# Optimization experiments

Measured on AMD Instinct MI355X. Metric: run time of the kernel, lower is better.

The kernel has to match this reference:

```python
import jax, jax.numpy as jnp
import numpy as np

N = 262144          # nodes
E = N * 16          # edges (avg degree 16)
C_IN = 64
C_OUT = 64
GRID = 0.5          # voxel size
POS_EXTENT = 10.0   # pos in [0, 10)^3
NVOX_DIM = int(round(POS_EXTENT / GRID))  # 20
NVOX = NVOX_DIM ** 3                      # 8000 voxels
BN_EPS = 1e-5


def setup_inputs() -> dict:
    key = jax.random.key(0)
    k = jax.random.split(key, 5)
    x = jax.random.normal(k[0], (N, C_IN), dtype=jnp.float32)
    pos = jax.random.uniform(k[1], (N, 3), dtype=jnp.float32, minval=0.0, maxval=POS_EXTENT)
    edge_index = jax.random.randint(k[2], (2, E), 0, N, dtype=jnp.int32)
    W = jax.random.normal(k[3], (C_IN, C_OUT), dtype=jnp.float32) / np.float32(np.sqrt(C_IN))
    b = jnp.zeros((C_OUT,), jnp.float32)
    gamma = jnp.ones((C_OUT,), jnp.float32)
    beta = jnp.zeros((C_OUT,), jnp.float32)
    return {"x": x, "pos": pos, "edge_index": edge_index,
            "W": W, "b": b, "gamma": gamma, "beta": beta}


def reference(x, pos, edge_index, W, b, gamma, beta):
    # --- self.down: Linear -> BatchNorm1d (training-mode batch stats) -> ReLU ---
    h = x @ W + b                                   # [N, C_OUT]
    mean = jnp.mean(h, axis=0)
    var = jnp.mean(jnp.square(h - mean), axis=0)    # biased variance (torch BN)
    h = (h - mean) * jax.lax.rsqrt(var + BN_EPS) * gamma + beta
    h = jax.nn.relu(h)

    # --- max_pool_neighbor_x: scatter-max of neighbor features (self-loops added) ---
    row, col = edge_index[0], edge_index[1]
    pooled = jax.ops.segment_max(h[row], col, num_segments=N)  # [N, C_OUT]
    h = jnp.maximum(pooled, h)  # self-loop; also fixes -inf for isolated nodes

    # --- GridSampling: voxel-grid quantize + per-voxel mean of x and pos ---
    vid = jnp.clip(jnp.floor(pos / GRID).astype(jnp.int32), 0, NVOX_DIM - 1)  # [N,3]
    vox = (vid[:, 0] * NVOX_DIM + vid[:, 1]) * NVOX_DIM + vid[:, 2]           # [N]
    cnt = jax.ops.segment_sum(jnp.ones((N,), jnp.float32), vox, num_segments=NVOX)
    x_sum = jax.ops.segment_sum(h, vox, num_segments=NVOX)     # [NVOX, C_OUT]
    p_sum = jax.ops.segment_sum(pos, vox, num_segments=NVOX)   # [NVOX, 3]
    denom = jnp.maximum(cnt, 1.0)[:, None]
    x_out = x_sum / denom
    pos_out = p_sum / denom
    # concat features and positions of the downsampled graph: [NVOX, C_OUT+3]
    return jnp.concatenate([x_out, pos_out], axis=1)
```

## Files before the change

### kernel.cpp

```cpp
#include <hip/hip_runtime.h>
#include <hip/hip_fp16.h>

#define NVOX_DIM 20
#define NVOX 8000
#define BN_EPS 1e-5f

#define NBUCK 2048
#define BSHIFT 7
#define NODES_PER_BUCK 128
#define GEMM_BLOCKS 1024
#define ZERO_BLOCKS 16
#define CAP 2560

typedef _Float16 f16x8 __attribute__((ext_vector_type(8)));
typedef float f32x4 __attribute__((ext_vector_type(4)));

__device__ __forceinline__ unsigned short f2key(float v) {
    unsigned short hb = __half_as_ushort(__float2half(v));
    unsigned short m = (unsigned short)(0x8000u | (unsigned short)(-(int)(hb >> 15)));
    return (unsigned short)(hb ^ m);
}

__global__ __launch_bounds__(256) void k0_fused(const float* __restrict__ x,
                                                const float* __restrict__ W,
                                                const float* __restrict__ bias,
                                                unsigned short* __restrict__ h16,
                                                float* __restrict__ partials, int n16,
                                                float4* __restrict__ zero_zone,
                                                int zero_n4) {
    __shared__ float sW[4096];
    __shared__ float red[2][4][64];
    int t = threadIdx.x;

    if (blockIdx.x >= GEMM_BLOCKS) {
        int zb = blockIdx.x - GEMM_BLOCKS;
        float4 z = {0.f, 0.f, 0.f, 0.f};
        for (int i = zb * 256 + t; i < zero_n4; i += ZERO_BLOCKS * 256) zero_zone[i] = z;
        return;
    }

    for (int i = t; i < 4096; i += 256) sW[i] = W[i];
    __syncthreads();
    int lane = t & 63;
    int w = t >> 6;
    int l15 = lane & 15;
    int q = lane >> 4;

    f16x8 bf[4][2];
#pragma unroll
    for (int t4 = 0; t4 < 4; ++t4)
#pragma unroll
        for (int kb = 0; kb < 2; ++kb)
#pragma unroll
            for (int i = 0; i < 8; ++i)
                bf[t4][kb][i] = (_Float16)sW[(kb * 32 + q * 8 + i) * 64 + t4 * 16 + l15];
    float bv[4];
#pragma unroll
    for (int t4 = 0; t4 < 4; ++t4) bv[t4] = bias[t4 * 16 + l15];

    float s[4] = {0.f, 0.f, 0.f, 0.f}, s2[4] = {0.f, 0.f, 0.f, 0.f};

    for (int g = blockIdx.x * 4 + w; g < n16; g += GEMM_BLOCKS * 4) {
        int row0 = g * 16;
        const float* xp = x + (size_t)(row0 + l15) * 64 + q * 8;
        float4 xa = *(const float4*)(xp);
        float4 xb = *(const float4*)(xp + 4);
        float4 xc = *(const float4*)(xp + 32);
        float4 xd = *(const float4*)(xp + 36);
        f16x8 a0, a1;
        a0[0] = (_Float16)xa.x; a0[1] = (_Float16)xa.y; a0[2] = (_Float16)xa.z; a0[3] = (_Float16)xa.w;
        a0[4] = (_Float16)xb.x; a0[5] = (_Float16)xb.y; a0[6] = (_Float16)xb.z; a0[7] = (_Float16)xb.w;
        a1[0] = (_Float16)xc.x; a1[1] = (_Float16)xc.y; a1[2] = (_Float16)xc.z; a1[3] = (_Float16)xc.w;
        a1[4] = (_Float16)xd.x; a1[5] = (_Float16)xd.y; a1[6] = (_Float16)xd.z; a1[7] = (_Float16)xd.w;

#pragma unroll
        for (int t4 = 0; t4 < 4; ++t4) {
            f32x4 acc = {bv[t4], bv[t4], bv[t4], bv[t4]};
            acc = __builtin_amdgcn_mfma_f32_16x16x32_f16(a0, bf[t4][0], acc, 0, 0, 0);
            acc = __builtin_amdgcn_mfma_f32_16x16x32_f16(a1, bf[t4][1], acc, 0, 0, 0);
            s[t4] += acc[0] + acc[1] + acc[2] + acc[3];
            s2[t4] = fmaf(acc[0], acc[0], s2[t4]);
            s2[t4] = fmaf(acc[1], acc[1], s2[t4]);
            s2[t4] = fmaf(acc[2], acc[2], s2[t4]);
            s2[t4] = fmaf(acc[3], acc[3], s2[t4]);
#pragma unroll
            for (int r = 0; r < 4; ++r) {
                h16[(size_t)(row0 + q * 4 + r) * 64 + t4 * 16 + l15] = f2key(acc[r]);
            }
        }
    }

#pragma unroll
    for (int t4 = 0; t4 < 4; ++t4) {
        s[t4] += __shfl_xor(s[t4], 16, 64);
        s[t4] += __shfl_xor(s[t4], 32, 64);
        s2[t4] += __shfl_xor(s2[t4], 16, 64);
        s2[t4] += __shfl_xor(s2[t4], 32, 64);
    }
    if (lane < 16) {
#pragma unroll
        for (int t4 = 0; t4 < 4; ++t4) {
            red[0][w][t4 * 16 + lane] = s[t4];
            red[1][w][t4 * 16 + lane] = s2[t4];
        }
    }
    __syncthreads();
    if (t < 128) {
        int c = t & 63;
        int which = t >> 6;
        float v = red[which][0][c] + red[which][1][c] + red[which][2][c] + red[which][3][c];
        partials[(size_t)blockIdx.x * 128 + which * 64 + c] = v;
    }
}

__global__ __launch_bounds__(1024) void k3_finalize(const float* __restrict__ partials,
                                                    const float* __restrict__ gamma,
                                                    const float* __restrict__ beta,
                                                    float* __restrict__ stats2, float invN) {
    __shared__ float red[8][128];
    __shared__ float tot[128];
    int t = threadIdx.x;
    int c = t & 127;
    int g = t >> 7;
    float s = 0.f;
    for (int b = g; b < GEMM_BLOCKS; b += 8) s += partials[(size_t)b * 128 + c];
    red[g][c] = s;
    __syncthreads();
    if (t < 128) {
        float v = 0.f;
#pragma unroll
        for (int g2 = 0; g2 < 8; ++g2) v += red[g2][t];
        tot[t] = v;
    }
    __syncthreads();
    if (t < 64) {
        float mean = tot[t] * invN;
        float var = tot[64 + t] * invN - mean * mean;
        float sc = gamma[t] * rsqrtf(var + BN_EPS);
        stats2[t] = sc;
        stats2[64 + t] = beta[t] - mean * sc;
    }
}

__global__ __launch_bounds__(1024) void k_bin(const int* __restrict__ rows,
                                              const int* __restrict__ cols,
                                              int* __restrict__ cursor,
                                              unsigned int* __restrict__ pairs, int E) {
    __shared__ int lh[NBUCK];
    __shared__ int lpos[NBUCK];
    int t = threadIdx.x;
    lh[t] = 0;
    lh[t + 1024] = 0;
    __syncthreads();
    int base = blockIdx.x * 16384 + t * 16;
    int r[16], c[16];
#pragma unroll
    for (int g4 = 0; g4 < 4; ++g4) {
        int e = base + g4 * 4;
        int4 r4 = *(const int4*)(rows + e);
        int4 c4 = *(const int4*)(cols + e);
        r[g4 * 4 + 0] = r4.x; c[g4 * 4 + 0] = c4.x;
        r[g4 * 4 + 1] = r4.y; c[g4 * 4 + 1] = c4.y;
        r[g4 * 4 + 2] = r4.z; c[g4 * 4 + 2] = c4.z;
        r[g4 * 4 + 3] = r4.w; c[g4 * 4 + 3] = c4.w;
    }
#pragma unroll
    for (int i = 0; i < 16; ++i) atomicAdd(&lh[c[i] >> BSHIFT], 1);
    __syncthreads();
    lpos[t] = atomicAdd(&cursor[t], lh[t]);
    lpos[t + 1024] = atomicAdd(&cursor[t + 1024], lh[t + 1024]);
    __syncthreads();
#pragma unroll
    for (int i = 0; i < 16; ++i) {
        int bkt = c[i] >> BSHIFT;
        int idx = atomicAdd(&lpos[bkt], 1);
        if (idx < CAP)
            pairs[(size_t)bkt * CAP + idx] =
                ((unsigned int)r[i] << BSHIFT) |
                (unsigned int)(c[i] & (NODES_PER_BUCK - 1));
    }
}

__global__ __launch_bounds__(512) void k_pool(const unsigned int* __restrict__ pairs,
                                              const int* __restrict__ cursor,
                                              const unsigned short* __restrict__ h16,
                                              const float* __restrict__ pos,
                                              const float* __restrict__ stats2,
                                              float* __restrict__ xs,
                                              float* __restrict__ ps,
                                              float* __restrict__ cnt) {
    __shared__ unsigned int tile[NODES_PER_BUCK * 64];
    int b = blockIdx.x;
    int t = threadIdx.x;
    int lane = t & 63;
    int w = t >> 6;
    float scale = stats2[lane];
    float shift = stats2[64 + lane];

    const unsigned int* src = (const unsigned int*)(h16 + (size_t)b * (NODES_PER_BUCK * 64));
#pragma unroll
    for (int k = 0; k < 8; ++k) {
        int i = t + k * 512;
        unsigned int u = src[i];
        tile[2 * i] = u & 0xFFFFu;
        tile[2 * i + 1] = u >> 16;
    }
    __syncthreads();

    int cntE = min(__builtin_amdgcn_readfirstlane(cursor[b]), CAP);
    int chunk = (((cntE + 7) >> 3) + 7) & ~7;
    int wu = __builtin_amdgcn_readfirstlane(w);
    int start = b * CAP;
    int cs = start + wu * chunk;
    int ce = min(cs + chunk, start + cntE);
    int j = cs;
    for (; j + 16 <= ce; j += 16) {
        uint4 qa = *(const uint4*)(pairs + j);
        uint4 qb = *(const uint4*)(pairs + j + 4);
        uint4 qc = *(const uint4*)(pairs + j + 8);
        uint4 qd = *(const uint4*)(pairs + j + 12);
        unsigned int v0 = h16[(size_t)(qa.x >> BSHIFT) * 64 + lane];
        unsigned int v1 = h16[(size_t)(qa.y >> BSHIFT) * 64 + lane];
        unsigned int v2 = h16[(size_t)(qa.z >> BSHIFT) * 64 + lane];
        unsigned int v3 = h16[(size_t)(qa.w >> BSHIFT) * 64 + lane];
        unsigned int v4 = h16[(size_t)(qb.x >> BSHIFT) * 64 + lane];
        unsigned int v5 = h16[(size_t)(qb.y >> BSHIFT) * 64 + lane];
        unsigned int v6 = h16[(size_t)(qb.z >> BSHIFT) * 64 + lane];
        unsigned int v7 = h16[(size_t)(qb.w >> BSHIFT) * 64 + lane];
        unsigned int v8 = h16[(size_t)(qc.x >> BSHIFT) * 64 + lane];
        unsigned int v9 = h16[(size_t)(qc.y >> BSHIFT) * 64 + lane];
        unsigned int va = h16[(size_t)(qc.z >> BSHIFT) * 64 + lane];
        unsigned int vb = h16[(size_t)(qc.w >> BSHIFT) * 64 + lane];
        unsigned int vc = h16[(size_t)(qd.x >> BSHIFT) * 64 + lane];
        unsigned int vd = h16[(size_t)(qd.y >> BSHIFT) * 64 + lane];
        unsigned int ve = h16[(size_t)(qd.z >> BSHIFT) * 64 + lane];
        unsigned int vf = h16[(size_t)(qd.w >> BSHIFT) * 64 + lane];
        const unsigned int M = NODES_PER_BUCK - 1;
        atomicMax(&tile[((qa.x & M) << 6) + lane], v0);
        atomicMax(&tile[((qa.y & M) << 6) + lane], v1);
        atomicMax(&tile[((qa.z & M) << 6) + lane], v2);
        atomicMax(&tile[((qa.w & M) << 6) + lane], v3);
        atomicMax(&tile[((qb.x & M) << 6) + lane], v4);
        atomicMax(&tile[((qb.y & M) << 6) + lane], v5);
        atomicMax(&tile[((qb.z & M) << 6) + lane], v6);
        atomicMax(&tile[((qb.w & M) << 6) + lane], v7);
        atomicMax(&tile[((qc.x & M) << 6) + lane], v8);
        atomicMax(&tile[((qc.y & M) << 6) + lane], v9);
        atomicMax(&tile[((qc.z & M) << 6) + lane], va);
        atomicMax(&tile[((qc.w & M) << 6) + lane], vb);
        atomicMax(&tile[((qd.x & M) << 6) + lane], vc);
        atomicMax(&tile[((qd.y & M) << 6) + lane], vd);
        atomicMax(&tile[((qd.z & M) << 6) + lane], ve);
        atomicMax(&tile[((qd.w & M) << 6) + lane], vf);
    }
    for (; j < ce; ++j) {
        unsigned int qq = __builtin_amdgcn_readfirstlane(pairs[j]);
        unsigned int v = h16[(size_t)(qq >> BSHIFT) * 64 + lane];
        atomicMax(&tile[((qq & (NODES_PER_BUCK - 1)) << 6) + lane], v);
    }
    __syncthreads();

#pragma unroll
    for (int nl = 0; nl < NODES_PER_BUCK; nl += 8) {
        int node_l = nl + w;
        int c = (b << BSHIFT) + node_l;
        float px = pos[(size_t)c * 3 + 0];
        float py = pos[(size_t)c * 3 + 1];
        float pz = pos[(size_t)c * 3 + 2];
        int v0 = min(max((int)floorf(px * 2.f), 0), NVOX_DIM - 1);
        int v1 = min(max((int)floorf(py * 2.f), 0), NVOX_DIM - 1);
        int v2 = min(max((int)floorf(pz * 2.f), 0), NVOX_DIM - 1);
        int vox = (v0 * NVOX_DIM + v1) * NVOX_DIM + v2;
        unsigned int k = tile[(node_l << 6) + lane];
        unsigned short hb = (k & 0x8000u) ? (unsigned short)(k ^ 0x8000u)
                                          : (unsigned short)(0xFFFFu ^ k);
        __half_raw hr;
        hr.x = hb;
        float v = __half2float((__half)hr);
        float val = fmaxf(fmaf(v, scale, shift), 0.f);
        atomicAdd(&xs[(size_t)vox * 64 + lane], val);
        if (lane < 3) atomicAdd(&ps[vox * 3 + lane], lane == 0 ? px : (lane == 1 ? py : pz));
        if (lane == 0) atomicAdd(&cnt[vox], 1.f);
    }
}

__global__ __launch_bounds__(256) void k7_out(const float* __restrict__ xs,
                                              const float* __restrict__ ps,
                                              const float* __restrict__ cnt,
                                              float* __restrict__ out, int total) {
    int idx = blockIdx.x * blockDim.x + threadIdx.x;
    if (idx >= total) return;
    int v = idx / 67;
    int c = idx - v * 67;
    float d = fmaxf(cnt[v], 1.f);
    float val = (c < 64) ? xs[(size_t)v * 64 + c] : ps[v * 3 + (c - 64)];
    out[idx] = val / d;
}

extern "C" void kernel_launch(void* const* d_in, const int* in_sizes, int n_in,
                              void* d_out, int out_size, void* d_ws, size_t ws_size,
                              hipStream_t stream) {
    const float* x     = (const float*)d_in[0];
    const float* pos   = (const float*)d_in[1];
    const int*   ei    = (const int*)d_in[2];
    const float* W     = (const float*)d_in[3];
    const float* b     = (const float*)d_in[4];
    const float* gamma = (const float*)d_in[5];
    const float* beta  = (const float*)d_in[6];
    float* out = (float*)d_out;

    const int n = in_sizes[0] / 64;
    const int E = in_sizes[2] / 2;

    char* ws = (char*)d_ws;
    unsigned short* h16      = (unsigned short*)(ws + 0);
    unsigned int*   pairs    = (unsigned int*)(ws + 33554432);
    float*          partials = (float*)(ws + 54525952);
    float*          stats2   = (float*)(ws + 55050240);
    int*            cursor   = (int*)(ws + 55051264);
    float*          xs       = (float*)(ws + 55059456);
    float*          ps       = (float*)(ws + 57107456);
    float*          cnt      = (float*)(ws + 57203456);
    float4*         zero4    = (float4*)(ws + 55059456);
    const int zero_n4 = (57235456 - 55059456) / 16;

    hipMemsetAsync(cursor, 0, NBUCK * 4, stream);

    k0_fused<<<GEMM_BLOCKS + ZERO_BLOCKS, 256, 0, stream>>>(x, W, b, h16, partials,
                                                            n >> 4, zero4, zero_n4);
    k_bin<<<E / 16384, 1024, 0, stream>>>(ei, ei + E, cursor, pairs, E);
    k3_finalize<<<1, 1024, 0, stream>>>(partials, gamma, beta, stats2, 1.0f / (float)n);
    k_pool<<<NBUCK, 512, 0, stream>>>(pairs, cursor, h16, pos, stats2, xs, ps, cnt);
    k7_out<<<(out_size + 255) / 256, 256, 0, stream>>>(xs, ps, cnt, out, out_size);
}
```

Measured before the change: 357.6 us.

## Replace voxel atomic scatter with per-voxel node lists and gather reduction

Nodes are binned into fixed-capacity per-voxel lists inside the edge-binning kernel. The pooling kernel now writes pooled fp16 keys to a buffer. A new per-voxel kernel then gathers those keys, applies BN and ReLU, and writes the averaged output directly. This removes float atomics to the voxel sums, the zeroing pass and the final divide kernel. Edge buckets also grow to 256 nodes with 1024-thread pool blocks. Two risks: the CAPV=96 limit silently drops nodes in crowded voxels (the mean is about 33 per voxel), and pooled results make an extra round trip through memory.

New measurement: 350.4 us. 2.0% less time.

```diff
diff --git a/kernel.cpp b/kernel.cpp
--- a/kernel.cpp
+++ b/kernel.cpp
@@ -5,12 +5,13 @@
 #define NVOX 8000
 #define BN_EPS 1e-5f
 
-#define NBUCK 2048
-#define BSHIFT 7
-#define NODES_PER_BUCK 128
+#define NBUCK 1024
+#define BSHIFT 8
+#define NODES_PER_BUCK 256
 #define GEMM_BLOCKS 1024
-#define ZERO_BLOCKS 16
-#define CAP 2560
+#define CAP 5120
+#define CAPV 96
+#define NODEBIN_BLOCKS 32
 
 typedef _Float16 f16x8 __attribute__((ext_vector_type(8)));
 typedef float f32x4 __attribute__((ext_vector_type(4)));
@@ -21,24 +22,22 @@
     return (unsigned short)(hb ^ m);
 }
 
-__global__ __launch_bounds__(256) void k0_fused(const float* __restrict__ x,
-                                                const float* __restrict__ W,
-                                                const float* __restrict__ bias,
-                                                unsigned short* __restrict__ h16,
-                                                float* __restrict__ partials, int n16,
-                                                float4* __restrict__ zero_zone,
-                                                int zero_n4) {
+__device__ __forceinline__ float key2f(unsigned int k) {
+    unsigned short hb = (k & 0x8000u) ? (unsigned short)(k ^ 0x8000u)
+                                      : (unsigned short)(0xFFFFu ^ k);
+    __half_raw hr;
+    hr.x = hb;
+    return __half2float((__half)hr);
+}
+
+__global__ __launch_bounds__(256) void k0_gemm(const float* __restrict__ x,
+                                               const float* __restrict__ W,
+                                               const float* __restrict__ bias,
+                                               unsigned short* __restrict__ h16,
+                                               float* __restrict__ partials, int n16) {
     __shared__ float sW[4096];
     __shared__ float red[2][4][64];
     int t = threadIdx.x;
-
-    if (blockIdx.x >= GEMM_BLOCKS) {
-        int zb = blockIdx.x - GEMM_BLOCKS;
-        float4 z = {0.f, 0.f, 0.f, 0.f};
-        for (int i = zb * 256 + t; i < zero_n4; i += ZERO_BLOCKS * 256) zero_zone[i] = z;
-        return;
-    }
-
     for (int i = t; i < 4096; i += 256) sW[i] = W[i];
     __syncthreads();
     int lane = t & 63;
@@ -144,13 +143,35 @@
 
 __global__ __launch_bounds__(1024) void k_bin(const int* __restrict__ rows,
                                               const int* __restrict__ cols,
-                                              int* __restrict__ cursor,
-                                              unsigned int* __restrict__ pairs, int E) {
+                                              const float* __restrict__ pos,
+                                              int* __restrict__ cursorE,
+                                              unsigned int* __restrict__ pairs,
+                                              int* __restrict__ cursorV,
+                                              int* __restrict__ vox_nodes,
+                                              int E, int n) {
     __shared__ int lh[NBUCK];
     __shared__ int lpos[NBUCK];
     int t = threadIdx.x;
+
+    if (blockIdx.x >= 256) {
+        int nb = blockIdx.x - 256;
+#pragma unroll
+        for (int i = 0; i < 8; ++i) {
+            int node = nb * 8192 + i * 1024 + t;
+            float px = pos[(size_t)node * 3 + 0];
+            float py = pos[(size_t)node * 3 + 1];
+            float pz = pos[(size_t)node * 3 + 2];
+            int v0 = min(max((int)floorf(px * 2.f), 0), NVOX_DIM - 1);
+            int v1 = min(max((int)floorf(py * 2.f), 0), NVOX_DIM - 1);
+            int v2 = min(max((int)floorf(pz * 2.f), 0), NVOX_DIM - 1);
+            int vox = (v0 * NVOX_DIM + v1) * NVOX_DIM + v2;
+            int idx = atomicAdd(&cursorV[vox], 1);
+            if (idx < CAPV) vox_nodes[vox * CAPV + idx] = node;
+        }
+        return;
+    }
+
     lh[t] = 0;
-    lh[t + 1024] = 0;
     __syncthreads();
     int base = blockIdx.x * 16384 + t * 16;
     int r[16], c[16];
@@ -167,8 +188,7 @@
 #pragma unroll
     for (int i = 0; i < 16; ++i) atomicAdd(&lh[c[i] >> BSHIFT], 1);
     __syncthreads();
-    lpos[t] = atomicAdd(&cursor[t], lh[t]);
-    lpos[t + 1024] = atomicAdd(&cursor[t + 1024], lh[t + 1024]);
+    lpos[t] = atomicAdd(&cursorE[t], lh[t]);
     __syncthreads();
 #pragma unroll
     for (int i = 0; i < 16; ++i) {
@@ -181,39 +201,34 @@
     }
 }
 
-__global__ __launch_bounds__(512) void k_pool(const unsigned int* __restrict__ pairs,
-                                              const int* __restrict__ cursor,
-                                              const unsigned short* __restrict__ h16,
-                                              const float* __restrict__ pos,
-                                              const float* __restrict__ stats2,
-                                              float* __restrict__ xs,
-                                              float* __restrict__ ps,
-                                              float* __restrict__ cnt) {
+__global__ __launch_bounds__(1024) void k_pool(const unsigned int* __restrict__ pairs,
+                                               const int* __restrict__ cursorE,
+                                               const unsigned short* __restrict__ h16,
+                                               unsigned short* __restrict__ pooled16) {
     __shared__ unsigned int tile[NODES_PER_BUCK * 64];
     int b = blockIdx.x;
     int t = threadIdx.x;
     int lane = t & 63;
     int w = t >> 6;
-    float scale = stats2[lane];
-    float shift = stats2[64 + lane];
 
     const unsigned int* src = (const unsigned int*)(h16 + (size_t)b * (NODES_PER_BUCK * 64));
 #pragma unroll
     for (int k = 0; k < 8; ++k) {
-        int i = t + k * 512;
+        int i = t + k * 1024;
         unsigned int u = src[i];
         tile[2 * i] = u & 0xFFFFu;
         tile[2 * i + 1] = u >> 16;
     }
     __syncthreads();
 
-    int cntE = min(__builtin_amdgcn_readfirstlane(cursor[b]), CAP);
-    int chunk = (((cntE + 7) >> 3) + 7) & ~7;
+    int cntE = min(__builtin_amdgcn_readfirstlane(cursorE[b]), CAP);
+    int chunk = (((cntE + 15) >> 4) + 7) & ~7;
     int wu = __builtin_amdgcn_readfirstlane(w);
     int start = b * CAP;
     int cs = start + wu * chunk;
     int ce = min(cs + chunk, start + cntE);
     int j = cs;
+    const unsigned int M = NODES_PER_BUCK - 1;
     for (; j + 16 <= ce; j += 16) {
         uint4 qa = *(const uint4*)(pairs + j);
         uint4 qb = *(const uint4*)(pairs + j + 4);
@@ -235,7 +250,6 @@
         unsigned int vd = h16[(size_t)(qd.y >> BSHIFT) * 64 + lane];
         unsigned int ve = h16[(size_t)(qd.z >> BSHIFT) * 64 + lane];
         unsigned int vf = h16[(size_t)(qd.w >> BSHIFT) * 64 + lane];
-        const unsigned int M = NODES_PER_BUCK - 1;
         atomicMax(&tile[((qa.x & M) << 6) + lane], v0);
         atomicMax(&tile[((qa.y & M) << 6) + lane], v1);
         atomicMax(&tile[((qa.z & M) << 6) + lane], v2);
@@ -256,45 +270,63 @@
     for (; j < ce; ++j) {
         unsigned int qq = __builtin_amdgcn_readfirstlane(pairs[j]);
         unsigned int v = h16[(size_t)(qq >> BSHIFT) * 64 + lane];
-        atomicMax(&tile[((qq & (NODES_PER_BUCK - 1)) << 6) + lane], v);
-    }
-    __syncthreads();
-
-#pragma unroll
-    for (int nl = 0; nl < NODES_PER_BUCK; nl += 8) {
+        atomicMax(&tile[((qq & M) << 6) + lane], v);
+    }
+    __syncthreads();
+
+#pragma unroll
+    for (int nl = 0; nl < NODES_PER_BUCK; nl += 16) {
         int node_l = nl + w;
-        int c = (b << BSHIFT) + node_l;
-        float px = pos[(size_t)c * 3 + 0];
-        float py = pos[(size_t)c * 3 + 1];
-        float pz = pos[(size_t)c * 3 + 2];
-        int v0 = min(max((int)floorf(px * 2.f), 0), NVOX_DIM - 1);
-        int v1 = min(max((int)floorf(py * 2.f), 0), NVOX_DIM - 1);
-        int v2 = min(max((int)floorf(pz * 2.f), 0), NVOX_DIM - 1);
-        int vox = (v0 * NVOX_DIM + v1) * NVOX_DIM + v2;
-        unsigned int k = tile[(node_l << 6) + lane];
-        unsigned short hb = (k & 0x8000u) ? (unsigned short)(k ^ 0x8000u)
-                                          : (unsigned short)(0xFFFFu ^ k);
-        __half_raw hr;
-        hr.x = hb;
-        float v = __half2float((__half)hr);
-        float val = fmaxf(fmaf(v, scale, shift), 0.f);
-        atomicAdd(&xs[(size_t)vox * 64 + lane], val);
-        if (lane < 3) atomicAdd(&ps[vox * 3 + lane], lane == 0 ? px : (lane == 1 ? py : pz));
-        if (lane == 0) atomicAdd(&cnt[vox], 1.f);
-    }
-}
-
-__global__ __launch_bounds__(256) void k7_out(const float* __restrict__ xs,
-                                              const float* __restrict__ ps,
-                                              const float* __restrict__ cnt,
-                                              float* __restrict__ out, int total) {
-    int idx = blockIdx.x * blockDim.x + threadIdx.x;
-    if (idx >= total) return;
-    int v = idx / 67;
-    int c = idx - v * 67;
-    float d = fmaxf(cnt[v], 1.f);
-    float val = (c < 64) ? xs[(size_t)v * 64 + c] : ps[v * 3 + (c - 64)];
-    out[idx] = val / d;
+        pooled16[((size_t)b * NODES_PER_BUCK + node_l) * 64 + lane] =
+            (unsigned short)tile[(node_l << 6) + lane];
+    }
+}
+
+__global__ __launch_bounds__(256) void k_vox(const int* __restrict__ vox_nodes,
+                                             const int* __restrict__ cursorV,
+                                             const unsigned short* __restrict__ pooled16,
+                                             const float* __restrict__ pos,
+                                             const float* __restrict__ stats2,
+                                             float* __restrict__ out) {
+    int t = threadIdx.x;
+    int lane = t & 63;
+    int w = t >> 6;
+    int vox = blockIdx.x * 4 + w;
+    float scale = stats2[lane];
+    float shift = stats2[64 + lane];
+    int cv = min(__builtin_amdgcn_readfirstlane(cursorV[vox]), CAPV);
+    int base = vox * CAPV;
+    float sum = 0.f;
+    float psum = 0.f;
+    int i = 0;
+    for (; i + 4 <= cv; i += 4) {
+        int4 nd = *(const int4*)(vox_nodes + base + i);
+        int n0 = __builtin_amdgcn_readfirstlane(nd.x);
+        int n1 = __builtin_amdgcn_readfirstlane(nd.y);
+        int n2 = __builtin_amdgcn_readfirstlane(nd.z);
+        int n3 = __builtin_amdgcn_readfirstlane(nd.w);
+        unsigned int k0 = pooled16[(size_t)n0 * 64 + lane];
+        unsigned int k1 = pooled16[(size_t)n1 * 64 + lane];
+        unsigned int k2 = pooled16[(size_t)n2 * 64 + lane];
+        unsigned int k3 = pooled16[(size_t)n3 * 64 + lane];
+        sum += fmaxf(fmaf(key2f(k0), scale, shift), 0.f);
+        sum += fmaxf(fmaf(key2f(k1), scale, shift), 0.f);
+        sum += fmaxf(fmaf(key2f(k2), scale, shift), 0.f);
+        sum += fmaxf(fmaf(key2f(k3), scale, shift), 0.f);
+        if (lane < 3) {
+            psum += pos[(size_t)n0 * 3 + lane] + pos[(size_t)n1 * 3 + lane] +
+                    pos[(size_t)n2 * 3 + lane] + pos[(size_t)n3 * 3 + lane];
+        }
+    }
+    for (; i < cv; ++i) {
+        int n0 = __builtin_amdgcn_readfirstlane(vox_nodes[base + i]);
+        unsigned int k0 = pooled16[(size_t)n0 * 64 + lane];
+        sum += fmaxf(fmaf(key2f(k0), scale, shift), 0.f);
+        if (lane < 3) psum += pos[(size_t)n0 * 3 + lane];
+    }
+    float inv = 1.f / fmaxf((float)cv, 1.f);
+    out[(size_t)vox * 67 + lane] = sum * inv;
+    if (lane < 3) out[(size_t)vox * 67 + 64 + lane] = psum * inv;
 }
 
 extern "C" void kernel_launch(void* const* d_in, const int* in_sizes, int n_in,
@@ -315,21 +347,19 @@
     char* ws = (char*)d_ws;
     unsigned short* h16      = (unsigned short*)(ws + 0);
     unsigned int*   pairs    = (unsigned int*)(ws + 33554432);
-    float*          partials = (float*)(ws + 54525952);
-    float*          stats2   = (float*)(ws + 55050240);
-    int*            cursor   = (int*)(ws + 55051264);
-    float*          xs       = (float*)(ws + 55059456);
-    float*          ps       = (float*)(ws + 57107456);
-    float*          cnt      = (float*)(ws + 57203456);
-    float4*         zero4    = (float4*)(ws + 55059456);
-    const int zero_n4 = (57235456 - 55059456) / 16;
-
-    hipMemsetAsync(cursor, 0, NBUCK * 4, stream);
-
-    k0_fused<<<GEMM_BLOCKS + ZERO_BLOCKS, 256, 0, stream>>>(x, W, b, h16, partials,
-                                                            n >> 4, zero4, zero_n4);
-    k_bin<<<E / 16384, 1024, 0, stream>>>(ei, ei + E, cursor, pairs, E);
+    unsigned short* pooled16 = (unsigned short*)(ws + 54525952);
+    float*          partials = (float*)(ws + 88080384);
+    float*          stats2   = (float*)(ws + 88604672);
+    int*            cursorE  = (int*)(ws + 88605696);
+    int*            cursorV  = (int*)(ws + 88609792);
+    int*            vox_nodes= (int*)(ws + 88642560);
+
+    hipMemsetAsync(cursorE, 0, 4096 + 32768, stream);
+
+    k0_gemm<<<GEMM_BLOCKS, 256, 0, stream>>>(x, W, b, h16, partials, n >> 4);
+    k_bin<<<256 + NODEBIN_BLOCKS, 1024, 0, stream>>>(ei, ei + E, pos, cursorE, pairs,
+                                                     cursorV, vox_nodes, E, n);
     k3_finalize<<<1, 1024, 0, stream>>>(partials, gamma, beta, stats2, 1.0f / (float)n);
-    k_pool<<<NBUCK, 512, 0, stream>>>(pairs, cursor, h16, pos, stats2, xs, ps, cnt);
-    k7_out<<<(out_size + 255) / 256, 256, 0, stream>>>(xs, ps, cnt, out, out_size);
-}
+    k_pool<<<NBUCK, 1024, 0, stream>>>(pairs, cursorE, h16, pooled16);
+    k_vox<<<NVOX / 4, 256, 0, stream>>>(vox_nodes, cursorV, pooled16, pos, stats2, out);
+}
```
